# Performance work log

Hardware: AMD Instinct MI355X
Metric: run time of the kernel (lower is better)

Reference implementation:

```python
import jax, jax.numpy as jnp
import numpy as np

N_HEADS = 12
HIDDEN = 768
HEAD_DIM = HIDDEN // N_HEADS
B, S = 4, 2048


def setup_inputs() -> dict:
    key = jax.random.key(0)
    ks = jax.random.split(key, 7)
    bound = 1.0 / np.sqrt(HIDDEN)  # torch nn.Linear default init range
    inputs = jax.random.normal(ks[0], (B, S, HIDDEN), dtype=jnp.float32)
    Wq = jax.random.uniform(ks[1], (HIDDEN, HIDDEN), jnp.float32, -bound, bound)
    bq = jax.random.uniform(ks[2], (HIDDEN,), jnp.float32, -bound, bound)
    Wk = jax.random.uniform(ks[3], (HIDDEN, HIDDEN), jnp.float32, -bound, bound)
    bk = jax.random.uniform(ks[4], (HIDDEN,), jnp.float32, -bound, bound)
    Wv = jax.random.uniform(ks[5], (HIDDEN, HIDDEN), jnp.float32, -bound, bound)
    bv = jax.random.uniform(ks[6], (HIDDEN,), jnp.float32, -bound, bound)
    return {"inputs": inputs, "Wq": Wq, "bq": bq, "Wk": Wk, "bk": bk, "Wv": Wv, "bv": bv}


def reference(inputs, Wq, bq, Wk, bk, Wv, bv):
    b, s, d = inputs.shape
    h, hd = N_HEADS, HEAD_DIM
    # torch Linear: x @ W^T + b; reshape to (b, s, h, hd) -> (b, h, s, hd)
    def proj(W, bias):
        y = inputs @ W.T + bias
        return y.reshape(b, s, h, hd).transpose(0, 2, 1, 3)
    q = proj(Wq, bq)
    k = proj(Wk, bk)
    v = proj(Wv, bv)
    scale = 1.0 / jnp.sqrt(jnp.asarray(hd, inputs.dtype))
    scores = jnp.einsum('bhqd,bhkd->bhqk', q, k) * scale  # [b,h,s,s] materialized as in source
    attn = jax.nn.softmax(scores, axis=-1)
    out = jnp.einsum('bhqk,bhkd->bhqd', attn, v)
    # (b, h, s, hd) -> (b, s, h*hd)
    return out.transpose(0, 2, 1, 3).reshape(b, s, d)
```

## Files before the change

kernel.cpp:

```cpp
#include <hip/hip_runtime.h>
#include <hip/hip_bf16.h>
#include <math.h>

#define NH   12
#define HD   64
#define HID  768
#define NB   4
#define SS   2048
#define MR   (NB*SS)

#define NXE  (MR*HID)
#define NWE  (HID*HID)

typedef unsigned short u16;
typedef u16   u16x8  __attribute__((ext_vector_type(8)));
typedef __bf16 bf16x8 __attribute__((ext_vector_type(8)));
typedef float f32x4  __attribute__((ext_vector_type(4)));

__device__ __forceinline__ u16 f2b(float f) {
    union { float f; unsigned i; } c; c.f = f;
    unsigned x = c.i + 0x7fffu + ((c.i >> 16) & 1u);
    return (u16)(x >> 16);
}
__device__ __forceinline__ unsigned pk2(float lo, float hi) {
    float2 f; f.x = lo; f.y = hi;
    union { __hip_bfloat162 h; unsigned u; } c;
    c.h = __float22bfloat162_rn(f);
    return c.u;
}
__device__ __forceinline__ f32x4 mfma16(u16x8 a, u16x8 b, f32x4 c) {
    return __builtin_amdgcn_mfma_f32_16x16x32_bf16(
        __builtin_bit_cast(bf16x8, a), __builtin_bit_cast(bf16x8, b), c, 0, 0, 0);
}
__device__ __forceinline__ void g2l16(const u16* g, u16* l) {
    __builtin_amdgcn_global_load_lds(
        (const __attribute__((address_space(1))) void*)g,
        (__attribute__((address_space(3))) void*)l, 16, 0, 0);
}
__device__ __forceinline__ int kperm(int k) {
    return ((k >> 5) << 5) | (((k >> 2) & 1) << 4) | (((k >> 3) & 3) << 2) | (k & 3);
}


__global__ __launch_bounds__(256) void to_bf16(
    const float* __restrict__ x,  const float* __restrict__ Wq,
    const float* __restrict__ Wk, const float* __restrict__ Wv,
    u16* __restrict__ dst)
{
    const int NX4 = NXE / 4, NW4 = NWE / 4, NT4 = NX4 + 3 * NW4;
    for (int i = blockIdx.x * 256 + threadIdx.x; i < NT4; i += gridDim.x * 256) {
        const float* src; u16* d;
        if (i < NX4) { src = x + (size_t)i * 4; d = dst + (size_t)i * 4; }
        else {
            int j = i - NX4; int w = j / NW4; int r = j - w * NW4;
            const float* Ws = (w == 0) ? Wq : ((w == 1) ? Wk : Wv);
            src = Ws + (size_t)r * 4; d = dst + NXE + (size_t)w * NWE + (size_t)r * 4;
        }
        float4 f = *(const float4*)src;
        uint2 o; o.x = pk2(f.x, f.y); o.y = pk2(f.z, f.w);
        *(uint2*)d = o;
    }
}

__global__ __launch_bounds__(256, 3) void qkv_proj(
    const u16* __restrict__ xb, const u16* __restrict__ Wb,
    const float* __restrict__ bq, const float* __restrict__ bk,
    const float* __restrict__ bv, u16* __restrict__ qkv)
{
    const int wsel = blockIdx.z;
    const u16* W = Wb + (size_t)wsel * NWE;
    const float* bias = (wsel == 0) ? bq : ((wsel == 1) ? bk : bv);
    u16* out = qkv + (size_t)wsel * MR * HID;

    const int m0 = blockIdx.x * 128, n0 = blockIdx.y * 128;
    __shared__ __align__(16) u16 smem[18432];

    const int tid  = threadIdx.x;
    const int lane = tid & 63, wid = tid >> 6;
    const int quad = lane >> 4, l16 = lane & 15;
    const int wm = wid >> 1, wn = wid & 1;
    const int qsw = quad ^ ((l16 >> 1) & 3);

    const int rA = 2 * wid * 16 + (lane >> 2);
    const int colh = 8 * ((lane & 3) ^ ((lane >> 3) & 3));
    const u16* gx0 = xb + (size_t)(m0 + rA) * HID + colh;
    const u16* gx1 = gx0 + (size_t)16 * HID;
    const u16* gw0 = W  + (size_t)(n0 + rA) * HID + colh;
    const u16* gw1 = gw0 + (size_t)16 * HID;
    u16* lA = smem + (2 * wid) * 512 + lane * 8;

    f32x4 acc[4][4] = {};

    for (int k0 = 0; k0 < HID; k0 += 64) {
        g2l16(gx0 + k0,      lA);            g2l16(gx1 + k0,      lA + 512);
        g2l16(gx0 + k0 + 32, lA + 4096);     g2l16(gx1 + k0 + 32, lA + 4608);
        g2l16(gw0 + k0,      lA + 8192);     g2l16(gw1 + k0,      lA + 8704);
        g2l16(gw0 + k0 + 32, lA + 12288);    g2l16(gw1 + k0 + 32, lA + 12800);
        __syncthreads();
        #pragma unroll
        for (int hh = 0; hh < 2; hh++) {
            u16x8 af[4], bf[4];
            #pragma unroll
            for (int i = 0; i < 4; i++)
                af[i] = *(const u16x8*)(smem + hh * 4096 + (wm * 64 + i * 16 + l16) * 32 + qsw * 8);
            #pragma unroll
            for (int j = 0; j < 4; j++)
                bf[j] = *(const u16x8*)(smem + 8192 + hh * 4096 + (wn * 64 + j * 16 + l16) * 32 + qsw * 8);
            #pragma unroll
            for (int i = 0; i < 4; i++)
                #pragma unroll
                for (int j = 0; j < 4; j++)
                    acc[i][j] = mfma16(af[i], bf[j], acc[i][j]);
        }
        __syncthreads();
    }

    if (wsel == 2) {
        u16* lt = smem + wid * 4608;
        #pragma unroll
        for (int j = 0; j < 4; j++) {
            const int col = n0 + wn * 64 + j * 16 + l16;
            const float bb = bias[col];
            #pragma unroll
            for (int i = 0; i < 4; i++) {
                uint2 pk;
                pk.x = pk2(acc[i][j][0] + bb, acc[i][j][1] + bb);
                pk.y = pk2(acc[i][j][2] + bb, acc[i][j][3] + bb);
                *(uint2*)(lt + (j * 16 + l16) * 72 + i * 16 + quad * 4) = pk;
            }
        }
        __syncthreads();
        const int bidx = m0 >> 11;
        const int s0 = (m0 & 2047) + wm * 64;
        #pragma unroll
        for (int it = 0; it < 8; it++) {
            const int dl = it * 8 + (lane >> 3), sl = (lane & 7) * 8;
            uint4 w = *(const uint4*)(lt + dl * 72 + sl);
            const int col = n0 + wn * 64 + dl;
            const int hh = col >> 6, d = col & 63;
            *(uint4*)(out + ((size_t)(bidx * NH + hh) * HD + d) * SS + s0 + sl) = w;
        }
    } else {
        const float scale = (wsel == 0) ? 0.18033688f : 1.0f;
        #pragma unroll
        for (int j = 0; j < 4; j++) {
            const int col = n0 + wn * 64 + j * 16 + l16;
            const float bb = bias[col];
            #pragma unroll
            for (int i = 0; i < 4; i++)
                #pragma unroll
                for (int r = 0; r < 4; r++) {
                    int row = m0 + wm * 64 + i * 16 + quad * 4 + r;
                    if (wsel == 1) row = (row & ~63) | kperm(row & 63);
                    out[(size_t)row * HID + col] = f2b((acc[i][j][r] + bb) * scale);
                }
        }
    }
}

__global__ __launch_bounds__(256, 3) void attn(
    const u16* __restrict__ qkv, float* __restrict__ out)
{
    const int lin = blockIdx.x;
    const int rx  = lin & 7;
    const int gg  = lin >> 3;
    const int qt  = gg & 15;
    const int bh  = rx * 6 + (gg >> 4);
    const int b   = bh / NH, h = bh - b * NH;
    const int q0  = qt * 128;

    const u16* qb  = qkv + (size_t)b * SS * HID + h * HD;
    const u16* kb  = qkv + (size_t)MR * HID + (size_t)b * SS * HID + h * HD;
    const u16* vtb = qkv + (size_t)2 * MR * HID + ((size_t)(b * NH + h) * HD) * SS;
    float*     ob  = out + (size_t)b * SS * HID + h * HD;

    __shared__ __align__(16) u16 KS[2][2][2048];
    __shared__ __align__(16) u16 VS[2][2][2048];

    const int tid  = threadIdx.x;
    const int lane = tid & 63, wid = tid >> 6;
    const int quad = lane >> 4, l16 = lane & 15;
    const int qsw = quad ^ ((l16 >> 1) & 3);

    const int srow = 16 * wid + (lane >> 2);
    const int sc8  = 8 * ((lane & 3) ^ ((lane >> 3) & 3));
    const int ldst = wid * 512 + lane * 8;

    u16x8 qf[2][2];
    #pragma unroll
    for (int t = 0; t < 2; t++) {
        const int row = q0 + t * 64 + wid * 16 + l16;
        #pragma unroll
        for (int hh = 0; hh < 2; hh++)
            qf[t][hh] = *(const u16x8*)(qb + (size_t)row * HID + hh * 32 + quad * 8);
    }

    u16x8 ones;
    #pragma unroll
    for (int e = 0; e < 8; e++) ones[e] = 0x3F80;

    f32x4 o2[2][4] = {};
    f32x4 lacc[2] = {};

    {
        const u16* kg = kb + (size_t)srow * HID + sc8;
        const u16* vg = vtb + (size_t)srow * SS + sc8;
        g2l16(kg, &KS[0][0][0] + ldst);  g2l16(kg + 32, &KS[0][1][0] + ldst);
        g2l16(vg, &VS[0][0][0] + ldst);  g2l16(vg + 32, &VS[0][1][0] + ldst);
    }
    __syncthreads();

    for (int kt = 0; kt < SS / 64; kt++) {
        const int cur = kt & 1;

        if (kt < 31) {
            const int kn = (kt + 1) * 64;
            const u16* kg = kb + (size_t)(kn + srow) * HID + sc8;
            const u16* vg = vtb + (size_t)srow * SS + kn + sc8;
            g2l16(kg, &KS[cur ^ 1][0][0] + ldst);  g2l16(kg + 32, &KS[cur ^ 1][1][0] + ldst);
            g2l16(vg, &VS[cur ^ 1][0][0] + ldst);  g2l16(vg + 32, &VS[cur ^ 1][1][0] + ldst);
        }

        u16x8 kf[4][2];
        #pragma unroll
        for (int n = 0; n < 4; n++)
            #pragma unroll
            for (int hh = 0; hh < 2; hh++)
                kf[n][hh] = *(const u16x8*)(&KS[cur][hh][0] + (n * 16 + l16) * 32 + qsw * 8);

        unsigned pkd[2][4][2];
        __builtin_amdgcn_s_setprio(1);
        #pragma unroll
        for (int t = 0; t < 2; t++)
            #pragma unroll
            for (int n = 0; n < 4; n++) {
                f32x4 s = {-6.f, -6.f, -6.f, -6.f};
                s = mfma16(kf[n][0], qf[t][0], s);
                s = mfma16(kf[n][1], qf[t][1], s);
                const float p0 = __builtin_amdgcn_exp2f(s[0]);
                const float p1 = __builtin_amdgcn_exp2f(s[1]);
                const float p2 = __builtin_amdgcn_exp2f(s[2]);
                const float p3 = __builtin_amdgcn_exp2f(s[3]);
                pkd[t][n][0] = pk2(p0, p1);
                pkd[t][n][1] = pk2(p2, p3);
            }
        __builtin_amdgcn_s_setprio(0);

        u16x8 vf[4][2];
        #pragma unroll
        for (int n2 = 0; n2 < 4; n2++)
            #pragma unroll
            for (int hh = 0; hh < 2; hh++)
                vf[n2][hh] = *(const u16x8*)(&VS[cur][hh][0] + (n2 * 16 + l16) * 32 + qsw * 8);

        __builtin_amdgcn_s_setprio(1);
        #pragma unroll
        for (int t = 0; t < 2; t++) {
            union { u16x8 v; unsigned d[4]; } bf0, bf1;
            bf0.d[0] = pkd[t][0][0]; bf0.d[1] = pkd[t][0][1];
            bf0.d[2] = pkd[t][1][0]; bf0.d[3] = pkd[t][1][1];
            bf1.d[0] = pkd[t][2][0]; bf1.d[1] = pkd[t][2][1];
            bf1.d[2] = pkd[t][3][0]; bf1.d[3] = pkd[t][3][1];
            lacc[t] = mfma16(ones, bf0.v, lacc[t]);
            lacc[t] = mfma16(ones, bf1.v, lacc[t]);
            #pragma unroll
            for (int n2 = 0; n2 < 4; n2++) {
                o2[t][n2] = mfma16(vf[n2][0], bf0.v, o2[t][n2]);
                o2[t][n2] = mfma16(vf[n2][1], bf1.v, o2[t][n2]);
            }
        }
        __builtin_amdgcn_s_setprio(0);
        __syncthreads();
    }

    #pragma unroll
    for (int t = 0; t < 2; t++) {
        const float inv = 1.f / lacc[t][0];
        const int q = q0 + t * 64 + wid * 16 + l16;
        #pragma unroll
        for (int n2 = 0; n2 < 4; n2++) {
            f32x4 w = o2[t][n2];
            w[0] *= inv; w[1] *= inv; w[2] *= inv; w[3] *= inv;
            *(f32x4*)(ob + (size_t)q * HID + n2 * 16 + quad * 4) = w;
        }
    }
}

extern "C" void kernel_launch(void* const* d_in, const int* in_sizes, int n_in,
                              void* d_out, int out_size, void* d_ws, size_t ws_size,
                              hipStream_t stream) {
    const float* x  = (const float*)d_in[0];
    const float* Wq = (const float*)d_in[1];
    const float* bq = (const float*)d_in[2];
    const float* Wk = (const float*)d_in[3];
    const float* bk = (const float*)d_in[4];
    const float* Wv = (const float*)d_in[5];
    const float* bv = (const float*)d_in[6];
    float* out = (float*)d_out;
    u16* qkv = (u16*)d_ws;
    u16* cvt = (u16*)d_out;

    to_bf16<<<1024, 256, 0, stream>>>(x, Wq, Wk, Wv, cvt);

    dim3 gp(MR / 128, HID / 128, 3);
    qkv_proj<<<gp, 256, 0, stream>>>(cvt, cvt + NXE, bq, bk, bv, qkv);

    attn<<<768, 256, 0, stream>>>(qkv, out);
}
```

Baseline: 185.0 us.

## Stream V directly from global memory and triple-buffer K in LDS

Moves V fragment loads out of shared memory so they go straight from global memory into registers. K tiles are now staged through a three-deep LDS ring with prefetch distance two. A single barrier per iteration, guarded by explicit vmcnt waits, replaces the two-buffer scheme. This is meant to halve LDS traffic and per-thread async copies and to cut synchronisation stalls, at the cost of uncoalesced-ish direct global V reads whose latency now sits on the critical path, and manual vmcnt accounting that is fragile because the V register loads also count toward vmcnt.

```diff
diff --git a/kernel.cpp b/kernel.cpp
--- a/kernel.cpp
+++ b/kernel.cpp
@@ -174,8 +174,7 @@
     const u16* vtb = qkv + (size_t)2 * MR * HID + ((size_t)(b * NH + h) * HD) * SS;
     float*     ob  = out + (size_t)b * SS * HID + h * HD;
 
-    __shared__ __align__(16) u16 KS[2][2][2048];
-    __shared__ __align__(16) u16 VS[2][2][2048];
+    __shared__ __align__(16) u16 KS[3][2][2048];
 
     const int tid  = threadIdx.x;
     const int lane = tid & 63, wid = tid >> 6;
@@ -186,6 +185,15 @@
     const int sc8  = 8 * ((lane & 3) ^ ((lane >> 3) & 3));
     const int ldst = wid * 512 + lane * 8;
 
+    const u16* kg = kb + (size_t)srow * HID + sc8;
+    const u16* vg0 = vtb + (size_t)l16 * SS + quad * 8;
+
+#define ASTAGE(kt, bf_) do {                                            \
+        const u16* k_ = kg + (size_t)(kt) * 64 * HID;                   \
+        g2l16(k_,      &KS[(bf_)][0][0] + ldst);                        \
+        g2l16(k_ + 32, &KS[(bf_)][1][0] + ldst);                        \
+    } while (0)
+
     u16x8 qf[2][2];
     #pragma unroll
     for (int t = 0; t < 2; t++) {
@@ -202,24 +210,24 @@
     f32x4 o2[2][4] = {};
     f32x4 lacc[2] = {};
 
-    {
-        const u16* kg = kb + (size_t)srow * HID + sc8;
-        const u16* vg = vtb + (size_t)srow * SS + sc8;
-        g2l16(kg, &KS[0][0][0] + ldst);  g2l16(kg + 32, &KS[0][1][0] + ldst);
-        g2l16(vg, &VS[0][0][0] + ldst);  g2l16(vg + 32, &VS[0][1][0] + ldst);
-    }
-    __syncthreads();
+    ASTAGE(0, 0);
+    ASTAGE(1, 1);
 
     for (int kt = 0; kt < SS / 64; kt++) {
-        const int cur = kt & 1;
-
-        if (kt < 31) {
-            const int kn = (kt + 1) * 64;
-            const u16* kg = kb + (size_t)(kn + srow) * HID + sc8;
-            const u16* vg = vtb + (size_t)srow * SS + kn + sc8;
-            g2l16(kg, &KS[cur ^ 1][0][0] + ldst);  g2l16(kg + 32, &KS[cur ^ 1][1][0] + ldst);
-            g2l16(vg, &VS[cur ^ 1][0][0] + ldst);  g2l16(vg + 32, &VS[cur ^ 1][1][0] + ldst);
-        }
+        const int cur = kt % 3, nb = (kt + 2) % 3;
+
+        if (kt < 31) asm volatile("s_waitcnt vmcnt(2)" ::: "memory");
+        else         asm volatile("s_waitcnt vmcnt(0)" ::: "memory");
+        __builtin_amdgcn_s_barrier();
+
+        u16x8 vf[4][2];
+        #pragma unroll
+        for (int n2 = 0; n2 < 4; n2++)
+            #pragma unroll
+            for (int hh = 0; hh < 2; hh++)
+                vf[n2][hh] = *(const u16x8*)(vg0 + (size_t)(n2 * 16) * SS + kt * 64 + hh * 32);
+
+        if (kt + 2 < 32) ASTAGE(kt + 2, nb);
 
         u16x8 kf[4][2];
         #pragma unroll
@@ -246,13 +254,6 @@
             }
         __builtin_amdgcn_s_setprio(0);
 
-        u16x8 vf[4][2];
-        #pragma unroll
-        for (int n2 = 0; n2 < 4; n2++)
-            #pragma unroll
-            for (int hh = 0; hh < 2; hh++)
-                vf[n2][hh] = *(const u16x8*)(&VS[cur][hh][0] + (n2 * 16 + l16) * 32 + qsw * 8);
-
         __builtin_amdgcn_s_setprio(1);
         #pragma unroll
         for (int t = 0; t < 2; t++) {
@@ -270,8 +271,8 @@
             }
         }
         __builtin_amdgcn_s_setprio(0);
-        __syncthreads();
-    }
+    }
+#undef ASTAGE
 
     #pragma unroll
     for (int t = 0; t < 2; t++) {
```

After: 225.3 us. 21.8% more time.
